# Kernel optimization log

Measured on AMD Instinct MI355X. Metric: run time of the kernel, lower is better.

The kernel has to match this reference:

```python
import jax, jax.numpy as jnp
import numpy as np

TINY = 1e-15
EPS = 1e-6  # float32 eps from the torch module
C = 1.0
S = 1.0 / np.sqrt(C)
SQRTC = np.sqrt(C)


def _sinhc(z):
    # stable sinh(z)/z with small-argument Taylor branch
    y = jnp.sinh(z) / jnp.maximum(z, EPS)
    y0 = 1.0 + z * z / 6.0
    return jnp.where(jnp.abs(z) < EPS, y0, y)


def _beta(x):
    denom = jnp.sqrt(1.0 + C * jnp.sum(x * x, axis=-1, keepdims=True))
    return 1.0 / jnp.maximum(denom, TINY)


def _log0(y):
    s = jnp.linalg.norm(y, axis=-1, keepdims=True)
    coef = jnp.arcsinh(s / S) / jnp.maximum(s / S, EPS)
    return coef * y


def _exp0(v):
    r = jnp.linalg.norm(v, axis=-1, keepdims=True)
    coef = jnp.sinh(r / S) / jnp.maximum(r / S, EPS)
    return coef * v


def _proj_tan0(v, max_norm=20.0):
    r = jnp.maximum(jnp.linalg.norm(v, axis=-1, keepdims=True), EPS)
    return jnp.minimum(max_norm / r, 1.0) * v


def _pt_0_to_y(y, v):
    b = _beta(y)
    coef = C * b / (1.0 + b)
    dot = jnp.sum(y * v, axis=-1, keepdims=True)
    return v + coef * dot * y


def _gyro_add(x, y):
    b_x = _beta(x)
    b_y = _beta(y)
    s2 = S * S
    xy = jnp.sum(x * y, axis=-1, keepdims=True)
    coef = b_x / (1.0 + b_x) * (xy / s2) + (1.0 - b_y) / b_y
    return x + y + coef * x


def _exp_map(x, v):
    s2 = S * S
    x_norm2 = jnp.sum(x * x, axis=-1, keepdims=True)
    v_norm2 = jnp.sum(v * v, axis=-1, keepdims=True)
    dot_x_v = jnp.sum(x * v, axis=-1, keepdims=True)
    g_pvv = jnp.maximum(v_norm2 - dot_x_v * dot_x_v / (s2 + x_norm2), TINY)
    r_g = jnp.sqrt(g_pvv)
    b_x = _beta(x)
    coef1 = b_x / (1.0 + b_x)
    coef2 = -(C * b_x ** 3) / jnp.maximum(1.0 + b_x, TINY) ** 2
    dpi_v = coef1 * v + coef2 * dot_x_v * x
    lambda_x = (1.0 + b_x) / jnp.maximum(b_x, TINY)
    z_arg = jnp.clip(SQRTC * r_g, -20.0, 20.0)
    w = lambda_x * _sinhc(z_arg) * dpi_v
    return _gyro_add(x, w)


def setup_inputs() -> dict:
    key = jax.random.key(0)
    k1, k2, k3 = jax.random.split(key, 3)
    N, D_IN, D_OUT = 16384, 2048, 2048
    x = jax.random.normal(k1, (N, D_IN), dtype=jnp.float32)
    # weight scaled ~1/sqrt(d_in) so tangent norms stay in a sane hyperbolic range
    W = jax.random.normal(k2, (D_OUT, D_IN), dtype=jnp.float32) * (1.0 / np.sqrt(D_IN))
    b = jax.random.normal(k3, (D_OUT,), dtype=jnp.float32) * 0.01
    return {"x": x, "W": W, "b": b}


def reference(x, W, b):
    # PV fully-connected layer: log map -> linear -> exp map -> transported bias
    v = _log0(x)                 # [N, d_in] tangent at origin
    u = v @ W.T                  # [N, d_out]
    u = _proj_tan0(u)            # tangent norm clamp (max_norm=20)
    y = _exp0(u)                 # [N, d_out] PV point
    bt = _pt_0_to_y(y, b)        # parallel transport bias tangent 0 -> y
    out = _exp_map(y, bt)        # geodesic step (includes gyro_add)
    return out
```

## Files before the change

kernel.cpp:

```cpp
#include <hip/hip_runtime.h>
#include <stdint.h>

typedef __bf16 bf16_t;
typedef __bf16 bf16x8 __attribute__((ext_vector_type(8)));
typedef float floatx4 __attribute__((ext_vector_type(4)));
typedef float f32x4 __attribute__((ext_vector_type(4)));

#define N_ROWS 16384
#define D_IN   2048
#define D_OUT  2048
#define EPSF   1e-6f
#define TINYF  1e-15f

#define BM 256
#define BN 256
#define BK 64
#define NT 96

__device__ __forceinline__ void load_lds16(const void* g, void* l) {
    __builtin_amdgcn_global_load_lds(
        (const __attribute__((address_space(1))) unsigned int*)(const unsigned int*)g,
        (__attribute__((address_space(3))) unsigned int*)(unsigned int*)l,
        16, 0, 0);
}

__global__ __launch_bounds__(256) void pvfc_wsplit(
    const float* __restrict__ W, bf16_t* __restrict__ Wh, bf16_t* __restrict__ Wl)
{
    const size_t i = ((size_t)blockIdx.x * 256 + threadIdx.x) * 8;
    f32x4 a = *(const f32x4*)(W + i);
    f32x4 c = *(const f32x4*)(W + i + 4);
    float v[8] = {a.x, a.y, a.z, a.w, c.x, c.y, c.z, c.w};
    bf16x8 hv, lv;
#pragma unroll
    for (int j = 0; j < 8; ++j) {
        const bf16_t h = (bf16_t)v[j];
        hv[j] = h;
        lv[j] = (bf16_t)(v[j] - (float)h);
    }
    *(bf16x8*)(Wh + i) = hv;
    *(bf16x8*)(Wl + i) = lv;
}

__global__ __launch_bounds__(256) void pvfc_prologue(
    const float* __restrict__ x, bf16_t* __restrict__ Ap)
{
    __shared__ float red[4];
    const int row = blockIdx.x, tid = threadIdx.x;
    const int lane = tid & 63, wave = tid >> 6;

    const float* xr = x + (size_t)row * D_IN + tid * 8;
    f32x4 a = __builtin_nontemporal_load((const f32x4*)xr);
    f32x4 c = __builtin_nontemporal_load((const f32x4*)(xr + 4));
    float v[8] = {a.x, a.y, a.z, a.w, c.x, c.y, c.z, c.w};

    float s = 0.f;
#pragma unroll
    for (int i = 0; i < 8; ++i) s += v[i] * v[i];
#pragma unroll
    for (int off = 32; off > 0; off >>= 1) s += __shfl_down(s, off, 64);
    if (lane == 0) red[wave] = s;
    __syncthreads();
    const float s2  = red[0] + red[1] + red[2] + red[3];
    const float nrm = sqrtf(s2);
    const float coef = asinhf(nrm) / fmaxf(nrm, EPSF);

    bf16x8 hv, lv;
#pragma unroll
    for (int j = 0; j < 8; ++j) {
        const float vi = coef * v[j];
        const bf16_t h = (bf16_t)vi;
        hv[j] = h;
        lv[j] = (bf16_t)(vi - (float)h);
    }
    bf16_t* ar = Ap + (size_t)row * (2 * D_IN);
    *(bf16x8*)(ar + tid * 8)         = hv;
    *(bf16x8*)(ar + D_IN + tid * 8)  = lv;
}

#define BAR __builtin_amdgcn_s_barrier()
#define SCHED_FENCE __builtin_amdgcn_sched_barrier(0)
#define WAIT_VM0 do { asm volatile("s_waitcnt vmcnt(0)" ::: "memory"); \
                      __builtin_amdgcn_sched_barrier(0); } while (0)

#define LOAD_AH(buf, qm, AF)                                                   \
    _Pragma("unroll")                                                          \
    for (int i = 0; i < 4; ++i) {                                              \
        const int rA = wm * 128 + ((qm) * 4 + i) * 16 + m16;                   \
        _Pragma("unroll")                                                      \
        for (int ks = 0; ks < 2; ++ks)                                         \
            AF[i][ks] = *(const bf16x8*)&As[buf][rA * BK +                     \
                                                 (((ks * 4 + quad) ^ sw) * 8)];\
    }

#define LOAD_B(buf, qn, bq)                                                    \
    _Pragma("unroll")                                                          \
    for (int j = 0; j < 2; ++j) {                                              \
        const int rB = wn * 64 + ((qn) * 2 + j) * 16 + m16;                    \
        _Pragma("unroll")                                                      \
        for (int ks = 0; ks < 2; ++ks)                                         \
            bq[j][ks] = *(const bf16x8*)&Bs[buf][rB * BK +                     \
                                                 (((ks * 4 + quad) ^ sw) * 8)];\
    }

#define MFMA_Q(AF, BQ, qm, qn)                                                 \
    do {                                                                       \
        __builtin_amdgcn_s_setprio(1);                                         \
        _Pragma("unroll")                                                      \
        for (int ks = 0; ks < 2; ++ks)                                         \
            _Pragma("unroll")                                                  \
            for (int i = 0; i < 4; ++i)                                        \
                _Pragma("unroll")                                              \
                for (int j = 0; j < 2; ++j)                                    \
                    acc[(qm) * 4 + i][(qn) * 2 + j] =                          \
                        __builtin_amdgcn_mfma_f32_16x16x32_bf16(               \
                            AF[i][ks], BQ[j][ks],                              \
                            acc[(qm) * 4 + i][(qn) * 2 + j], 0, 0, 0);         \
        __builtin_amdgcn_s_setprio(0);                                         \
    } while (0)

#define TILE_BODY(rb, sb, st)                                                  \
    do {                                                                       \
        stageA(st, 0, sb); stageA(st, 1, sb);                                  \
        stageB(st, 0, sb); stageB(st, 1, sb);                                  \
        SCHED_FENCE;                                                           \
        LOAD_AH(rb, 0, afA); LOAD_B(rb, 0, bq0); LOAD_B(rb, 1, bq1);           \
        SCHED_FENCE;                                                           \
        MFMA_Q(afA, bq0, 0, 0);                                                \
        SCHED_FENCE;                                                           \
        LOAD_AH(rb, 1, afB);                                                   \
        SCHED_FENCE;                                                           \
        MFMA_Q(afA, bq1, 0, 1);                                                \
        MFMA_Q(afB, bq1, 1, 1);                                                \
        MFMA_Q(afB, bq0, 1, 0);                                                \
        WAIT_VM0;                                                              \
        BAR;                                                                   \
    } while (0)

__global__ __launch_bounds__(512, 2) void pvfc_gemm(
    const bf16_t* __restrict__ A,
    const bf16_t* __restrict__ Wh, const bf16_t* __restrict__ Wl,
    float* __restrict__ U)
{
    __shared__ __align__(16) bf16_t As[2][BM * BK];
    __shared__ __align__(16) bf16_t Bs[2][BN * BK];

    const int tid  = threadIdx.x;
    const int wave = tid >> 6, lane = tid & 63;
    const int bid  = blockIdx.x;
    const int colBase = (bid & 7) * BN;
    const int rowBase = (bid >> 3) * BM;

    const int wm = wave >> 2, wn = wave & 3;
    const int m16 = lane & 15, quad = lane >> 4;
    const int sw  = m16 & 7;

    const int sRow = tid >> 3;
    const int sCol = ((tid & 7) ^ (sRow & 7)) * 8;
    const int ldsOff = wave * 512;

    floatx4 acc[8][4];
    bf16x8 afA[4][2], afB[4][2], bq0[2][2], bq1[2][2];
    const floatx4 z = {0.f, 0.f, 0.f, 0.f};
#pragma unroll
    for (int i = 0; i < 8; ++i)
#pragma unroll
        for (int j = 0; j < 4; ++j) acc[i][j] = z;

    auto stageA = [&](int tile, int half, int buf) {
        const int tt  = tile < NT ? tile : NT - 1;
        const int seg = tt >> 5;
        const size_t off = (size_t)((seg == 1) ? D_IN : 0) + (size_t)(tt & 31) * BK;
        const bf16_t* src = A + (size_t)(rowBase + half * 128 + sRow) * (2 * D_IN)
                              + off + sCol;
        bf16_t* dst = &As[buf][half * 128 * BK + ldsOff];
        load_lds16(src, dst);
        load_lds16(src + (size_t)64 * (2 * D_IN), dst + 64 * BK);
    };
    auto stageB = [&](int tile, int half, int buf) {
        const int tt  = tile < NT ? tile : NT - 1;
        const bf16_t* Wp = ((tt >> 5) == 2) ? Wl : Wh;
        const int k0 = (tt & 31) * BK;
        const bf16_t* src = Wp + (size_t)(colBase + half * 128 + sRow) * D_IN
                               + k0 + sCol;
        bf16_t* dst = &Bs[buf][half * 128 * BK + ldsOff];
        load_lds16(src, dst);
        load_lds16(src + (size_t)64 * D_IN, dst + 64 * BK);
    };

    stageA(0, 0, 0); stageA(0, 1, 0); stageB(0, 0, 0); stageB(0, 1, 0);
    WAIT_VM0;
    BAR;

#pragma clang loop unroll(disable)
    for (int t = 0; t < NT; t += 2) {
        TILE_BODY(0, 1, t + 1);
        TILE_BODY(1, 0, t + 2);
    }

#pragma unroll
    for (int mi = 0; mi < 8; ++mi)
#pragma unroll
        for (int ni = 0; ni < 4; ++ni) {
            const int col = colBase + wn * 64 + ni * 16 + m16;
            float* up = U + (size_t)(rowBase + wm * 128 + mi * 16 + quad * 4) * D_OUT
                          + col;
#pragma unroll
            for (int r = 0; r < 4; ++r)
                __builtin_nontemporal_store(acc[mi][ni][r], up + (size_t)r * D_OUT);
        }
}

__global__ __launch_bounds__(256) void pvfc_epilogue(
    const float* __restrict__ U, const float* __restrict__ bvec,
    float* __restrict__ out)
{
    __shared__ float red[12];
    const int row = blockIdx.x, tid = threadIdx.x;
    const int lane = tid & 63, wave = tid >> 6;

    const float* ur = U + (size_t)row * D_OUT + tid * 8;
    float u[8];
    { f32x4 a = __builtin_nontemporal_load((const f32x4*)ur);
      f32x4 c = __builtin_nontemporal_load((const f32x4*)(ur + 4));
      u[0]=a.x;u[1]=a.y;u[2]=a.z;u[3]=a.w;u[4]=c.x;u[5]=c.y;u[6]=c.z;u[7]=c.w; }
    float b[8];
    { const float* br = bvec + tid * 8;
      f32x4 a = *(const f32x4*)br, c = *(const f32x4*)(br + 4);
      b[0]=a.x;b[1]=a.y;b[2]=a.z;b[3]=a.w;b[4]=c.x;b[5]=c.y;b[6]=c.z;b[7]=c.w; }

    float su2 = 0.f, sub = 0.f, sbb = 0.f;
#pragma unroll
    for (int i = 0; i < 8; ++i) { su2 += u[i]*u[i]; sub += u[i]*b[i]; sbb += b[i]*b[i]; }
#pragma unroll
    for (int off = 32; off > 0; off >>= 1) {
        su2 += __shfl_down(su2, off, 64);
        sub += __shfl_down(sub, off, 64);
        sbb += __shfl_down(sbb, off, 64);
    }
    if (lane == 0) { red[wave] = su2; red[4 + wave] = sub; red[8 + wave] = sbb; }
    __syncthreads();
    su2 = red[0] + red[1] + red[2] + red[3];
    sub = red[4] + red[5] + red[6] + red[7];
    sbb = red[8] + red[9] + red[10] + red[11];

    const float r0 = sqrtf(su2);
    const float t  = fminf(20.f / fmaxf(r0, EPSF), 1.f);
    const float rp = t * r0;
    const float coef_e = sinhf(rp) / fmaxf(rp, EPSF);
    const float P  = coef_e * t;
    const float yn2 = P * P * su2;
    const float beta = 1.f / fmaxf(sqrtf(1.f + yn2), TINYF);
    const float c  = beta / (1.f + beta);
    const float d  = P * sub;
    const float vn2   = sbb + c * d * d * (2.f + c * yn2);
    const float dotxv = d * (1.f + c * yn2);
    const float g  = fmaxf(vn2 - dotxv * dotxv / (1.f + yn2), TINYF);
    const float rg = sqrtf(g);
    const float coef1 = beta / (1.f + beta);
    const float t1 = fmaxf(1.f + beta, TINYF);
    const float coef2 = -(beta * beta * beta) / (t1 * t1);
    const float lam = (1.f + beta) / fmaxf(beta, TINYF);
    const float z  = fminf(rg, 20.f);
    const float sc = (fabsf(z) < EPSF) ? (1.f + z * z * (1.f / 6.f))
                                       : (sinhf(z) / fmaxf(z, EPSF));
    const float L = lam * sc;
    const float alpha = L * coef1;
    const float gamma = L * (coef1 * c * d + coef2 * dotxv);
    const float wn2 = alpha * alpha * sbb + 2.f * alpha * gamma * d + gamma * gamma * yn2;
    const float bw  = 1.f / fmaxf(sqrtf(1.f + wn2), TINYF);
    const float xy  = alpha * d + gamma * yn2;
    const float coefg = coef1 * xy + (1.f - bw) / bw;
    const float Ascale = P * (1.f + gamma + coefg);

    float* orow = out + (size_t)row * D_OUT + tid * 8;
    f32x4 o0, o1;
    o0.x = Ascale*u[0] + alpha*b[0]; o0.y = Ascale*u[1] + alpha*b[1];
    o0.z = Ascale*u[2] + alpha*b[2]; o0.w = Ascale*u[3] + alpha*b[3];
    o1.x = Ascale*u[4] + alpha*b[4]; o1.y = Ascale*u[5] + alpha*b[5];
    o1.z = Ascale*u[6] + alpha*b[6]; o1.w = Ascale*u[7] + alpha*b[7];
    __builtin_nontemporal_store(o0, (f32x4*)orow);
    __builtin_nontemporal_store(o1, (f32x4*)(orow + 4));
}

extern "C" void kernel_launch(void* const* d_in, const int* in_sizes, int n_in,
                              void* d_out, int out_size, void* d_ws, size_t ws_size,
                              hipStream_t stream)
{
    const float* x = (const float*)d_in[0];
    const float* W = (const float*)d_in[1];
    const float* b = (const float*)d_in[2];
    float* out = (float*)d_out;

    bf16_t* Wh = (bf16_t*)d_ws;
    bf16_t* Wl = Wh + (size_t)D_OUT * D_IN;
    char*   rest = (char*)(Wl + (size_t)D_OUT * D_IN);
    const size_t wbytes = (size_t)D_OUT * D_IN * 2 * 2;
    const size_t avail  = (ws_size > wbytes) ? ws_size - wbytes : 0;
    int chunk = (int)((avail / 16384 / 256) * 256);
    if (chunk <= 0) chunk = 256;
    if (chunk > N_ROWS) chunk = N_ROWS;

    bf16_t* Ap = (bf16_t*)rest;
    float*  U  = (float*)(rest + (size_t)chunk * (2 * D_IN) * 2);

    pvfc_wsplit<<<(D_OUT * D_IN) / (256 * 8), 256, 0, stream>>>(W, Wh, Wl);
    for (int r0 = 0; r0 < N_ROWS; r0 += chunk) {
        const int rows = (N_ROWS - r0 < chunk) ? (N_ROWS - r0) : chunk;
        pvfc_prologue<<<rows, 256, 0, stream>>>(x + (size_t)r0 * D_IN, Ap);
        pvfc_gemm<<<dim3(D_OUT / BN * (rows / BM)), 512, 0, stream>>>(Ap, Wh, Wl, U);
        pvfc_epilogue<<<rows, 256, 0, stream>>>(U, b, out + (size_t)r0 * D_OUT);
    }
}
```

Measured before the change: 635.5 us.

## Triple-buffer LDS with BK=32 and register double-buffered fragment prefetch

Restructures the GEMM main loop so that K tiles are halved to 32, shared memory becomes a three-stage ring buffer, and the A/B fragments for the next tile are read from LDS into a second register set while MFMAs run on the current set. The aim is to hide both global-to-LDS latency and LDS-read latency behind matrix math. The cost is twice as many barriers per unit of work, more registers, and no XOR swizzle on the LDS layout, which may cause bank conflicts.

```diff
diff --git a/kernel.cpp b/kernel.cpp
--- a/kernel.cpp
+++ b/kernel.cpp
@@ -14,8 +14,8 @@
 
 #define BM 256
 #define BN 256
-#define BK 64
-#define NT 96
+#define BK 32
+#define NT 192
 
 __device__ __forceinline__ void load_lds16(const void* g, void* l) {
     __builtin_amdgcn_global_load_lds(
@@ -80,59 +80,44 @@
 
 #define BAR __builtin_amdgcn_s_barrier()
 #define SCHED_FENCE __builtin_amdgcn_sched_barrier(0)
-#define WAIT_VM0 do { asm volatile("s_waitcnt vmcnt(0)" ::: "memory"); \
-                      __builtin_amdgcn_sched_barrier(0); } while (0)
-
-#define LOAD_AH(buf, qm, AF)                                                   \
+#define WAIT_LGKM0 do { asm volatile("s_waitcnt lgkmcnt(0)" ::: "memory"); \
+                        __builtin_amdgcn_sched_barrier(0); } while (0)
+#define WAIT_VM0   do { asm volatile("s_waitcnt vmcnt(0)" ::: "memory");   \
+                        __builtin_amdgcn_sched_barrier(0); } while (0)
+
+#define READ_A4(AF, brd, h)                                                    \
     _Pragma("unroll")                                                          \
     for (int i = 0; i < 4; ++i) {                                              \
-        const int rA = wm * 128 + ((qm) * 4 + i) * 16 + m16;                   \
-        _Pragma("unroll")                                                      \
-        for (int ks = 0; ks < 2; ++ks)                                         \
-            AF[i][ks] = *(const bf16x8*)&As[buf][rA * BK +                     \
-                                                 (((ks * 4 + quad) ^ sw) * 8)];\
-    }
-
-#define LOAD_B(buf, qn, bq)                                                    \
+        const int mi = (h) * 4 + i;                                            \
+        AF[mi] = *(const bf16x8*)&As3[(brd) * 8192 +                           \
+                    (wm * 128 + mi * 16 + m16) * 32 + quad * 8];               \
+    }
+#define READ_B4(BF, brd)                                                       \
     _Pragma("unroll")                                                          \
-    for (int j = 0; j < 2; ++j) {                                              \
-        const int rB = wn * 64 + ((qn) * 2 + j) * 16 + m16;                    \
-        _Pragma("unroll")                                                      \
-        for (int ks = 0; ks < 2; ++ks)                                         \
-            bq[j][ks] = *(const bf16x8*)&Bs[buf][rB * BK +                     \
-                                                 (((ks * 4 + quad) ^ sw) * 8)];\
-    }
-
-#define MFMA_Q(AF, BQ, qm, qn)                                                 \
+    for (int j = 0; j < 4; ++j)                                                \
+        BF[j] = *(const bf16x8*)&Bs3[(brd) * 8192 +                            \
+                    (wn * 64 + j * 16 + m16) * 32 + quad * 8];
+#define MFMA_G(AF, BF, g)                                                      \
     do {                                                                       \
         __builtin_amdgcn_s_setprio(1);                                         \
         _Pragma("unroll")                                                      \
-        for (int ks = 0; ks < 2; ++ks)                                         \
+        for (int i = 0; i < 2; ++i)                                            \
             _Pragma("unroll")                                                  \
-            for (int i = 0; i < 4; ++i)                                        \
-                _Pragma("unroll")                                              \
-                for (int j = 0; j < 2; ++j)                                    \
-                    acc[(qm) * 4 + i][(qn) * 2 + j] =                          \
-                        __builtin_amdgcn_mfma_f32_16x16x32_bf16(               \
-                            AF[i][ks], BQ[j][ks],                              \
-                            acc[(qm) * 4 + i][(qn) * 2 + j], 0, 0, 0);         \
+            for (int j = 0; j < 4; ++j)                                        \
+                acc[(g) * 2 + i][j] = __builtin_amdgcn_mfma_f32_16x16x32_bf16( \
+                    AF[(g) * 2 + i], BF[j], acc[(g) * 2 + i][j], 0, 0, 0);     \
         __builtin_amdgcn_s_setprio(0);                                         \
     } while (0)
 
-#define TILE_BODY(rb, sb, st)                                                  \
+#define BODY(AC, BC, AN, BN_, brd, bst, stT)                                   \
     do {                                                                       \
-        stageA(st, 0, sb); stageA(st, 1, sb);                                  \
-        stageB(st, 0, sb); stageB(st, 1, sb);                                  \
+        WAIT_LGKM0;                 \
+        stage_tile(stT, bst);                 \
         SCHED_FENCE;                                                           \
-        LOAD_AH(rb, 0, afA); LOAD_B(rb, 0, bq0); LOAD_B(rb, 1, bq1);           \
-        SCHED_FENCE;                                                           \
-        MFMA_Q(afA, bq0, 0, 0);                                                \
-        SCHED_FENCE;                                                           \
-        LOAD_AH(rb, 1, afB);                                                   \
-        SCHED_FENCE;                                                           \
-        MFMA_Q(afA, bq1, 0, 1);                                                \
-        MFMA_Q(afB, bq1, 1, 1);                                                \
-        MFMA_Q(afB, bq0, 1, 0);                                                \
+        READ_A4(AN, brd, 0); MFMA_G(AC, BC, 0); SCHED_FENCE;                   \
+        READ_A4(AN, brd, 1); MFMA_G(AC, BC, 1); SCHED_FENCE;                   \
+        READ_B4(BN_, brd);   MFMA_G(AC, BC, 2); SCHED_FENCE;                   \
+        MFMA_G(AC, BC, 3);                                                     \
         WAIT_VM0;                                                              \
         BAR;                                                                   \
     } while (0)
@@ -142,8 +127,8 @@
     const bf16_t* __restrict__ Wh, const bf16_t* __restrict__ Wl,
     float* __restrict__ U)
 {
-    __shared__ __align__(16) bf16_t As[2][BM * BK];
-    __shared__ __align__(16) bf16_t Bs[2][BN * BK];
+    __shared__ __align__(16) bf16_t As3[3 * BM * BK];
+    __shared__ __align__(16) bf16_t Bs3[3 * BN * BK];
 
     const int tid  = threadIdx.x;
     const int wave = tid >> 6, lane = tid & 63;
@@ -153,49 +138,47 @@
 
     const int wm = wave >> 2, wn = wave & 3;
     const int m16 = lane & 15, quad = lane >> 4;
-    const int sw  = m16 & 7;
-
-    const int sRow = tid >> 3;
-    const int sCol = ((tid & 7) ^ (sRow & 7)) * 8;
-    const int ldsOff = wave * 512;
 
     floatx4 acc[8][4];
-    bf16x8 afA[4][2], afB[4][2], bq0[2][2], bq1[2][2];
+    bf16x8 af0[8], af1[8], bf0[4], bf1[4];
     const floatx4 z = {0.f, 0.f, 0.f, 0.f};
 #pragma unroll
     for (int i = 0; i < 8; ++i)
 #pragma unroll
         for (int j = 0; j < 4; ++j) acc[i][j] = z;
 
-    auto stageA = [&](int tile, int half, int buf) {
+    const int sRow = tid >> 2;
+    const int sC   = (tid & 3) * 8;
+    auto stage_tile = [&](int tile, int b) {
         const int tt  = tile < NT ? tile : NT - 1;
-        const int seg = tt >> 5;
-        const size_t off = (size_t)((seg == 1) ? D_IN : 0) + (size_t)(tt & 31) * BK;
-        const bf16_t* src = A + (size_t)(rowBase + half * 128 + sRow) * (2 * D_IN)
-                              + off + sCol;
-        bf16_t* dst = &As[buf][half * 128 * BK + ldsOff];
-        load_lds16(src, dst);
-        load_lds16(src + (size_t)64 * (2 * D_IN), dst + 64 * BK);
+        const int seg = tt >> 6;
+        const int k0  = (tt & 63) * BK;
+        const size_t aOff = (size_t)((seg == 1) ? D_IN : 0) + k0;
+        const bf16_t* Wp  = (seg == 2) ? Wl : Wh;
+        bf16_t* da = As3 + b * 8192 + wave * 512;
+        bf16_t* db = Bs3 + b * 8192 + wave * 512;
+        load_lds16(A + (size_t)(rowBase + sRow) * (2 * D_IN) + aOff + sC, da);
+        load_lds16(A + (size_t)(rowBase + 128 + sRow) * (2 * D_IN) + aOff + sC,
+                   da + 4096);
+        load_lds16(Wp + (size_t)(colBase + sRow) * D_IN + k0 + sC, db);
+        load_lds16(Wp + (size_t)(colBase + 128 + sRow) * D_IN + k0 + sC,
+                   db + 4096);
     };
-    auto stageB = [&](int tile, int half, int buf) {
-        const int tt  = tile < NT ? tile : NT - 1;
-        const bf16_t* Wp = ((tt >> 5) == 2) ? Wl : Wh;
-        const int k0 = (tt & 31) * BK;
-        const bf16_t* src = Wp + (size_t)(colBase + half * 128 + sRow) * D_IN
-                               + k0 + sCol;
-        bf16_t* dst = &Bs[buf][half * 128 * BK + ldsOff];
-        load_lds16(src, dst);
-        load_lds16(src + (size_t)64 * D_IN, dst + 64 * BK);
-    };
-
-    stageA(0, 0, 0); stageA(0, 1, 0); stageB(0, 0, 0); stageB(0, 1, 0);
+
+    stage_tile(0, 0);
+    stage_tile(1, 1);
     WAIT_VM0;
     BAR;
+    READ_A4(af0, 0, 0); READ_A4(af0, 0, 1); READ_B4(bf0, 0);
 
 #pragma clang loop unroll(disable)
-    for (int t = 0; t < NT; t += 2) {
-        TILE_BODY(0, 1, t + 1);
-        TILE_BODY(1, 0, t + 2);
+    for (int t = 0; t < NT; t += 6) {
+        BODY(af0, bf0, af1, bf1, 1, 2, t + 2);
+        BODY(af1, bf1, af0, bf0, 2, 0, t + 3);
+        BODY(af0, bf0, af1, bf1, 0, 1, t + 4);
+        BODY(af1, bf1, af0, bf0, 1, 2, t + 5);
+        BODY(af0, bf0, af1, bf1, 2, 0, t + 6);
+        BODY(af1, bf1, af0, bf0, 0, 1, t + 7);
     }
 
 #pragma unroll
```

Measured after the change: 697.0 us. 1.1x slower.
